# Kernel optimization log

Measured on AMD Instinct MI355X. Metric: run time of the kernel, lower is better.

## Reference

```python
import jax, jax.numpy as jnp
import numpy as np

B, T, V, D, HD, NH, L, F, MD = 16, 512, 2048, 512, 64, 8, 6, 2048, 16


def setup_inputs() -> dict:
    key = jax.random.key(0)
    ks = jax.random.split(key, 12)
    s = 0.02
    def n(k, shape):
        return jax.random.normal(k, shape, jnp.float32) * s
    return {
        "idx": jax.random.randint(ks[0], (B, T), 0, V),
        "emb": n(ks[1], (V, D)),
        "Wq": n(ks[2], (L, D, HD)), "bq": jnp.zeros((L, HD), jnp.float32),
        "Wk": n(ks[3], (L, D, HD)), "bk": jnp.zeros((L, HD), jnp.float32),
        "Wv": n(ks[4], (L, D, HD)), "bv": jnp.zeros((L, HD), jnp.float32),
        "rel_table": n(ks[5], (L, 2 * MD + 1, HD)),
        "Wo": n(ks[6], (L, NH * HD, D)), "bo": jnp.zeros((L, D), jnp.float32),
        "g1": jnp.ones((L, D), jnp.float32), "be1": jnp.zeros((L, D), jnp.float32),
        "g2": jnp.ones((L, D), jnp.float32), "be2": jnp.zeros((L, D), jnp.float32),
        "W1": n(ks[7], (L, D, F)), "b1": jnp.zeros((L, F), jnp.float32),
        "W2": n(ks[8], (L, F, D)), "b2": jnp.zeros((L, D), jnp.float32),
        "Wout": n(ks[9], (D, V)), "bout": jnp.zeros((V,), jnp.float32),
    }


def _pos_encoding(t_len, d):
    # NOTE: replicates repo bug: exponent is 2*i/d with i already even.
    pos = jnp.arange(t_len, dtype=jnp.float32)[:, None]
    i = jnp.arange(0, d, 2, dtype=jnp.float32)[None, :]
    ang = pos / jnp.power(jnp.float32(10000.0), 2.0 * i / d)
    pe = jnp.zeros((t_len, d), jnp.float32)
    pe = pe.at[:, 0::2].set(jnp.sin(ang))
    pe = pe.at[:, 1::2].set(jnp.cos(ang))
    return pe


def _ln(x, g, b):
    m = jnp.mean(x, -1, keepdims=True)
    v = jnp.var(x, -1, keepdims=True)  # biased variance, as torch LayerNorm
    return (x - m) / jnp.sqrt(v + 1e-5) * g + b


def reference(idx, emb, Wq, bq, Wk, bk, Wv, bv, rel_table, Wo, bo,
              g1, be1, g2, be2, W1, b1, W2, b2, Wout, bout):
    t_len = idx.shape[1]
    x = emb[idx]                                   # [B,T,D]
    h = 2.0 * x + _pos_encoding(t_len, D)          # forward adds x + (x + pe)
    t = jnp.arange(t_len)
    dm = jnp.clip(t[None, :] - t[:, None], -MD, MD) + MD  # dm[a,b] = clamp(b-a)
    causal = t[:, None] >= t[None, :]
    scale = 1.0 / jnp.sqrt(jnp.float32(HD))
    neg_inf = jnp.float32(-jnp.inf)
    for l in range(L):
        y = _ln(h, g1[l], be1[l])
        Q = y @ Wq[l] + bq[l]                      # [B,T,HD]
        K = y @ Wk[l] + bk[l]
        Vv = y @ Wv[l] + bv[l]
        bias = rel_table[l][dm]                    # [T,T,HD]; k_bias == v_bias in source
        scores = jnp.einsum('bth,bsh->bts', Q, K)
        rel = jnp.einsum('bth,tsh->bts', Q, bias)
        att = jax.nn.softmax(jnp.where(causal, (scores + rel) * scale, neg_inf), axis=-1)
        vals = jnp.einsum('bts,bsh->bth', att, Vv) + jnp.einsum('bts,tsh->bth', att, bias)
        cat = jnp.tile(vals, (1, 1, NH))           # all NH heads share one module's weights
        h = h + cat @ Wo[l] + bo[l]
        y2 = _ln(h, g2[l], be2[l])
        h = h + jax.nn.relu(y2 @ W1[l] + b1[l]) @ W2[l] + b2[l]
    return h @ Wout + bout                         # [B,T,V]
```

## Files before the change

kernel.cpp:

```cpp
#include <hip/hip_runtime.h>
#include <hip/hip_bf16.h>
#include <math.h>

#define BB 16
#define TT 512
#define VV 2048
#define DD 512
#define HDD 64
#define LL 6
#define FF 2048
#define BT 8192

typedef __hip_bfloat16 bf16;
typedef __attribute__((ext_vector_type(8))) short bf8s;
typedef __attribute__((ext_vector_type(4))) float f4;

__device__ __forceinline__ float cvt(float x){ return x; }
__device__ __forceinline__ float cvt(bf16 x){ return __bfloat162float(x); }

__device__ __forceinline__ void gl16(const bf16* g, bf16* l){
  __builtin_amdgcn_global_load_lds(
      (const __attribute__((address_space(1))) void*)g,
      (__attribute__((address_space(3))) void*)l,
      16, 0, 0);
}

__global__ void k_flag(const void* g1, int* flagp){
  if(threadIdx.x==0 && blockIdx.x==0){
    const unsigned short* u = (const unsigned short*)g1;
    *flagp = (u[0] == 0) ? 1 : 0;
  }
}

__global__ __launch_bounds__(256) void k_cvt_all(
    const void* rel, const void* bo, const void* g1, const void* be1,
    const void* g2, const void* be2, const void* b1, const void* b2,
    const void* bout, const void* bq, const void* bk, const void* bv,
    bf16* d_rel, bf16* d_bo, bf16* d_g1, bf16* d_be1,
    bf16* d_g2, bf16* d_be2, bf16* d_b1, bf16* d_b2,
    bf16* d_bout, bf16* d_bqkv, const int* __restrict__ flagp){
  int i = blockIdx.x*256 + threadIdx.x;
  bool isf = *flagp;
  auto ld = [&](const void* s, int k)->float{
    return isf ? ((const float*)s)[k] : cvt(((const bf16*)s)[k]);
  };
  if(i < 12672){ d_rel[i] = (bf16)ld(rel, i); return; } i -= 12672;
  if(i < 3072){ d_bo[i]  = (bf16)ld(bo, i);  return; } i -= 3072;
  if(i < 3072){ d_g1[i]  = (bf16)ld(g1, i);  return; } i -= 3072;
  if(i < 3072){ d_be1[i] = (bf16)ld(be1, i); return; } i -= 3072;
  if(i < 3072){ d_g2[i]  = (bf16)ld(g2, i);  return; } i -= 3072;
  if(i < 3072){ d_be2[i] = (bf16)ld(be2, i); return; } i -= 3072;
  if(i < 12288){ d_b1[i] = (bf16)ld(b1, i);  return; } i -= 12288;
  if(i < 3072){ d_b2[i]  = (bf16)ld(b2, i);  return; } i -= 3072;
  if(i < 2048){ d_bout[i]= (bf16)ld(bout, i);return; } i -= 2048;
  if(i < 384){ int l=i>>6, hh=i&63; d_bqkv[l*192 + hh]       = (bf16)ld(bq, i); return; } i -= 384;
  if(i < 384){ int l=i>>6, hh=i&63; d_bqkv[l*192 + 64 + hh]  = (bf16)ld(bk, i); return; } i -= 384;
  if(i < 384){ int l=i>>6, hh=i&63; d_bqkv[l*192 + 128 + hh] = (bf16)ld(bv, i); return; }
}

__global__ __launch_bounds__(256) void k_tr(const void* __restrict__ src, bf16* __restrict__ dst,
                                            int R, int C, long long sS, long long sD, int ldD,
                                            const int* __restrict__ flagp){
  __shared__ bf16 t[32][33];
  int z = blockIdx.z;
  int c0 = blockIdx.x*32, r0 = blockIdx.y*32;
  int tx = threadIdx.x & 31, ty = threadIdx.x >> 5;
  bool isf = flagp && (*flagp);
  const float* sf = (const float*)src;
  const bf16*  sb = (const bf16*)src;
  for(int i=ty; i<32; i+=8){
    size_t off = (size_t)z*sS + (size_t)(r0+i)*C + (c0+tx);
    float v = isf ? sf[off] : cvt(sb[off]);
    t[i][tx] = (bf16)v;
  }
  __syncthreads();
  for(int i=ty; i<32; i+=8){
    dst[(size_t)z*sD + (size_t)(c0+i)*ldD + (r0+tx)] = t[tx][i];
  }
}

__global__ __launch_bounds__(256) void k_wsumT(const void* __restrict__ Wo,
                                               bf16* __restrict__ wsT,
                                               const int* __restrict__ flagp){
  int i = blockIdx.x*256 + threadIdx.x;
  if(i >= LL*64*512) return;
  int l = i >> 15, j = i & 32767, hh = j>>9, d = j&511;
  size_t loff = (size_t)l*512*512;
  bool isf = *flagp;
  float a = 0.f;
  #pragma unroll
  for(int n=0;n<8;++n){
    size_t idx = loff + (size_t)(n*64+hh)*512 + d;
    a += isf ? ((const float*)Wo)[idx] : cvt(((const bf16*)Wo)[idx]);
  }
  wsT[(size_t)l*32768 + d*64 + hh] = (bf16)a;
}

__global__ __launch_bounds__(256) void k_embed(const int* __restrict__ idx,
                                               const void* __restrict__ emb,
                                               float* __restrict__ h,
                                               const int* __restrict__ flagp){
  int r = blockIdx.x;
  int t = r & (TT-1);
  int tok = idx[r];
  bool isf = *flagp;
  for(int d = threadIdx.x; d < DD; d += 256){
    int p = d >> 1;
    float ang = (float)t * powf(10000.f, -(float)p * (1.f/128.f));
    float pe = (d & 1) ? cosf(ang) : sinf(ang);
    size_t off = (size_t)tok*DD + d;
    float ev = isf ? ((const float*)emb)[off] : cvt(((const bf16*)emb)[off]);
    h[(size_t)r*DD + d] = 2.f*ev + pe;
  }
}

__global__ __launch_bounds__(256) void k_ln(const float* __restrict__ x,
                                            const bf16* __restrict__ g,
                                            const bf16* __restrict__ b,
                                            bf16* __restrict__ y){
  int r = blockIdx.x;
  int tid = threadIdx.x;
  const float* xr = x + (size_t)r*DD;
  float v0 = xr[tid], v1 = xr[tid+256];
  float s = v0+v1, s2 = v0*v0 + v1*v1;
  for(int o=32;o;o>>=1){ s += __shfl_down(s,o); s2 += __shfl_down(s2,o); }
  __shared__ float red[8];
  int wv = tid>>6, ln = tid&63;
  if(ln==0){ red[wv]=s; red[4+wv]=s2; }
  __syncthreads();
  float a  = red[0]+red[1]+red[2]+red[3];
  float a2 = red[4]+red[5]+red[6]+red[7];
  float m  = a*(1.f/DD);
  float var = a2*(1.f/DD) - m*m;
  float inv = rsqrtf(var + 1e-5f);
  y[(size_t)r*DD+tid]     = (bf16)((v0-m)*inv*cvt(g[tid])     + cvt(b[tid]));
  y[(size_t)r*DD+tid+256] = (bf16)((v1-m)*inv*cvt(g[tid+256]) + cvt(b[tid+256]));
}

template<int BM,int BN,int WM,int WN,int CMODE,bool RELU,bool RESID,bool TRV>
__global__ __launch_bounds__(WM*WN*64) void mm(const bf16* __restrict__ A,
                                          const bf16* __restrict__ Bt,
                                          void* __restrict__ Cv,
                                          const bf16* __restrict__ bias,
                                          int M, int N, int K,
                                          long long sA, long long sB, long long sC, int sBias,
                                          int gx,
                                          const int* __restrict__ flagp,
                                          bf16* __restrict__ vtr){
  constexpr int BK  = 64;
  constexpr int NT  = WM*WN*64;
  constexpr int FM  = BM/(WM*16);
  constexpr int FN  = BN/(WN*16);
  constexpr int S   = (BM+BN)*BK;
  constexpr int CAW = (BM*BK/512)/(NT/64);
  constexpr int CBW = (BN*BK/512)/(NT/64);
  __shared__ bf16 lds[2*S];
  int nwg = gridDim.x, bid = blockIdx.x;
  int q = nwg>>3, rr = nwg&7, xcd = bid&7, ii = bid>>3;
  int wg = (xcd<rr ? xcd*(q+1) : rr*(q+1)+(xcd-rr)*q) + ii;
  int bx = wg % gx, by = wg / gx;
  int z = blockIdx.z;
  A  += (size_t)z*sA;
  Bt += (size_t)z*sB;
  if(bias) bias += (size_t)z*sBias;
  int tid = threadIdx.x, lane = tid&63, w = tid>>6;
  int m0 = by*BM, n0 = bx*BN;
  int wrow = (w/WN)*(FM*16), wcol = (w%WN)*(FN*16);
  int l15 = lane&15, l4 = lane>>4;
  int lrow = lane>>3, lgr = lane&7;
  int nk = K/BK;
  auto stage = [&](int kt, int buf){
    bf16* Ab = lds + buf*S;
    bf16* Bb = Ab + BM*BK;
    const bf16* gA = A + (size_t)m0*K + kt*BK;
    const bf16* gB = Bt + (size_t)n0*K + kt*BK;
    #pragma unroll
    for(int i=0;i<CAW;++i){
      int chunk = w*CAW + i;
      int row = chunk*8 + lrow;
      gl16(gA + (size_t)row*K + ((lgr ^ (row&7))*8), Ab + chunk*512);
    }
    #pragma unroll
    for(int i=0;i<CBW;++i){
      int chunk = w*CBW + i;
      int row = chunk*8 + lrow;
      gl16(gB + (size_t)row*K + ((lgr ^ (row&7))*8), Bb + chunk*512);
    }
  };
  f4 acc[FM][FN] = {};
  stage(0, 0);
  __syncthreads();
  for(int kt=0; kt<nk; ++kt){
    int cur = kt & 1;
    if(kt+1 < nk) stage(kt+1, cur^1);
    const bf16* Ab = lds + cur*S;
    const bf16* Bb = Ab + BM*BK;
    #pragma unroll
    for(int g=0; g<2; ++g){
      bf8s af[FM], bfv[FN];
      #pragma unroll
      for(int i=0;i<FM;++i){
        int r = wrow + i*16 + l15;
        af[i] = *(const bf8s*)(Ab + r*BK + (((g*4+l4) ^ (r&7))*8));
      }
      #pragma unroll
      for(int j=0;j<FN;++j){
        int r = wcol + j*16 + l15;
        bfv[j] = *(const bf8s*)(Bb + r*BK + (((g*4+l4) ^ (r&7))*8));
      }
      #pragma unroll
      for(int i=0;i<FM;++i)
        #pragma unroll
        for(int j=0;j<FN;++j)
          acc[i][j] = __builtin_amdgcn_mfma_f32_16x16x32_bf16(af[i], bfv[j], acc[i][j], 0,0,0);
    }
    __syncthreads();
  }
  bool f32o = (CMODE==2) ? (*flagp != 0) : (CMODE==1);
  bool trv = TRV && (z == 2);
  #pragma unroll
  for(int i=0;i<FM;++i){
    #pragma unroll
    for(int j=0;j<FN;++j){
      int col = n0 + wcol + j*16 + l15;
      float bv = bias ? cvt(bias[col]) : 0.f;
      #pragma unroll
      for(int q2=0;q2<4;++q2){
        int row = m0 + wrow + i*16 + l4*4 + q2;
        float v = acc[i][j][q2] + bv;
        if(trv){
          int b = row >> 9, t = row & 511;
          vtr[(size_t)b*(64*512) + (size_t)col*512 + t] = (bf16)v;
          continue;
        }
        size_t off = (size_t)z*sC + (size_t)row*N + col;
        if(RESID) v += ((const float*)Cv)[off];
        if(RELU)  v = fmaxf(v, 0.f);
        if(CMODE==0)      ((bf16*)Cv)[off] = (bf16)v;
        else if(CMODE==1) ((float*)Cv)[off] = v;
        else if(CMODE==3) vtr[off] = (bf16)v;
        else { if(f32o) ((float*)Cv)[off] = v; else ((bf16*)Cv)[off] = (bf16)v; }
      }
    }
  }
}

__global__ __launch_bounds__(256) void k_projln(const bf16* __restrict__ vals,
                                                const bf16* __restrict__ wsT,
                                                const bf16* __restrict__ bo,
                                                const bf16* __restrict__ g,
                                                const bf16* __restrict__ be,
                                                float* __restrict__ h,
                                                bf16* __restrict__ y){
  __shared__ bf16 Al[32*64];
  __shared__ bf16 Bl[512*64];
  __shared__ float rs[4][32], rs2[4][32];
  int m0 = blockIdx.x*32;
  int tid = threadIdx.x, lane = tid&63, w = tid>>6;
  int l15 = lane&15, l4 = lane>>4;
  int lrow = lane>>3, lgr = lane&7;
  {
    int row = w*8 + lrow;
    gl16(vals + (size_t)(m0+row)*64 + ((lgr ^ (row&7))*8), Al + w*512);
  }
  #pragma unroll
  for(int i=0;i<16;++i){
    int chunk = w*16 + i;
    int row = chunk*8 + lrow;
    gl16(wsT + (size_t)row*64 + ((lgr ^ (row&7))*8), Bl + chunk*512);
  }
  __syncthreads();
  int wcol = w*128;
  f4 acc[2][8] = {};
  #pragma unroll
  for(int g2=0; g2<2; ++g2){
    bf8s af[2], bfv[8];
    #pragma unroll
    for(int i=0;i<2;++i){
      int r = i*16 + l15;
      af[i] = *(const bf8s*)(Al + r*64 + (((g2*4+l4) ^ (r&7))*8));
    }
    #pragma unroll
    for(int j=0;j<8;++j){
      int r = wcol + j*16 + l15;
      bfv[j] = *(const bf8s*)(Bl + r*64 + (((g2*4+l4) ^ (r&7))*8));
    }
    #pragma unroll
    for(int i=0;i<2;++i)
      #pragma unroll
      for(int j=0;j<8;++j)
        acc[i][j] = __builtin_amdgcn_mfma_f32_16x16x32_bf16(af[i], bfv[j], acc[i][j], 0,0,0);
  }
  #pragma unroll
  for(int i=0;i<2;++i){
    float s[4] = {0,0,0,0}, s2[4] = {0,0,0,0};
    #pragma unroll
    for(int j=0;j<8;++j){
      int col = wcol + j*16 + l15;
      float bv = cvt(bo[col]);
      #pragma unroll
      for(int q=0;q<4;++q){
        int row = m0 + i*16 + l4*4 + q;
        size_t off = (size_t)row*512 + col;
        float v = acc[i][j][q] + bv + h[off];
        acc[i][j][q] = v;
        h[off] = v;
        s[q] += v; s2[q] += v*v;
      }
    }
    #pragma unroll
    for(int q=0;q<4;++q){
      #pragma unroll
      for(int o=1;o<16;o<<=1){ s[q] += __shfl_xor(s[q],o); s2[q] += __shfl_xor(s2[q],o); }
      if(l15==0){ rs[w][i*16+l4*4+q] = s[q]; rs2[w][i*16+l4*4+q] = s2[q]; }
    }
  }
  __syncthreads();
  #pragma unroll
  for(int i=0;i<2;++i){
    #pragma unroll
    for(int q=0;q<4;++q){
      int rloc = i*16 + l4*4 + q;
      float a  = rs[0][rloc]+rs[1][rloc]+rs[2][rloc]+rs[3][rloc];
      float a2 = rs2[0][rloc]+rs2[1][rloc]+rs2[2][rloc]+rs2[3][rloc];
      float mean = a*(1.f/512.f);
      float var  = a2*(1.f/512.f) - mean*mean;
      float inv  = rsqrtf(var + 1e-5f);
      int row = m0 + rloc;
      #pragma unroll
      for(int j=0;j<8;++j){
        int col = wcol + j*16 + l15;
        y[(size_t)row*512+col] = (bf16)((acc[i][j][q]-mean)*inv*cvt(g[col]) + cvt(be[col]));
      }
    }
  }
}

__global__ __launch_bounds__(256) void k_attn_fused(const bf16* __restrict__ Q,
                                                    const bf16* __restrict__ K,
                                                    const bf16* __restrict__ VbT,
                                                    const bf16* __restrict__ rel,
                                                    bf16* __restrict__ vals){
  int ti = blockIdx.x, b = blockIdx.y;
  int t0 = ti*16;
  int tid = threadIdx.x, lane = tid & 63, wc = tid >> 6;
  int l15 = lane & 15, l4 = lane >> 4;
  __shared__ bf16  Plds[16][520];
  __shared__ float qrs[16][17];
  __shared__ float amlds[16][17];
  __shared__ float redmx[4][16];
  __shared__ float redsum[4][16];
  int nj = ti + 1;
  int KC = (nj*16 + 31) >> 5;

  const bf16* Qb = Q + ((size_t)b*512 + t0)*64;
  const bf16* Kb = K + (size_t)b*512*64;
  const bf16* Vb = VbT + (size_t)b*64*512;

  for(int i=tid; i<16*17; i+=256) ((float*)amlds)[i] = 0.f;
  if(nj & 1) Plds[tid>>4][nj*16 + (tid&15)] = (bf16)0.f;

  bf8s af0 = *(const bf8s*)(Qb + (size_t)l15*64 + l4*8);
  bf8s af1 = *(const bf8s*)(Qb + (size_t)l15*64 + 32 + l4*8);

  if(wc < 2){
    f4 qa = {};
    bf8s r0 = *(const bf8s*)(rel + (size_t)(wc*16+l15)*64 + l4*8);
    bf8s r1 = *(const bf8s*)(rel + (size_t)(wc*16+l15)*64 + 32 + l4*8);
    qa = __builtin_amdgcn_mfma_f32_16x16x32_bf16(af0, r0, qa, 0,0,0);
    qa = __builtin_amdgcn_mfma_f32_16x16x32_bf16(af1, r1, qa, 0,0,0);
    int m = wc*16 + l15;
    if(m < 17){
      #pragma unroll
      for(int q=0;q<4;++q) qrs[l4*4+q][m] = qa[q];
    }
  }
  __syncthreads();

  float mx4[4] = {-INFINITY,-INFINITY,-INFINITY,-INFINITY};
  for(int j=wc; j<nj; j+=4){
    f4 sa = {};
    const bf16* kr = Kb + (size_t)(j*16+l15)*64;
    bf8s k0 = *(const bf8s*)(kr + l4*8);
    bf8s k1 = *(const bf8s*)(kr + 32 + l4*8);
    sa = __builtin_amdgcn_mfma_f32_16x16x32_bf16(af0, k0, sa, 0,0,0);
    sa = __builtin_amdgcn_mfma_f32_16x16x32_bf16(af1, k1, sa, 0,0,0);
    int s = j*16 + l15;
    #pragma unroll
    for(int q=0;q<4;++q){
      int row = l4*4+q, t = t0+row;
      float sp = -1e30f;
      if(s <= t){
        int m = s - t + 16; m = m < 0 ? 0 : m;
        sp = (sa[q] + qrs[row][m])*0.125f;
        mx4[q] = fmaxf(mx4[q], sp);
      }
      Plds[row][s] = (bf16)sp;
    }
  }
  #pragma unroll
  for(int q=0;q<4;++q){
    float m = mx4[q];
    m = fmaxf(m, __shfl_xor(m,1)); m = fmaxf(m, __shfl_xor(m,2));
    m = fmaxf(m, __shfl_xor(m,4)); m = fmaxf(m, __shfl_xor(m,8));
    mx4[q] = m;
  }
  if(l15==0){
    #pragma unroll
    for(int q=0;q<4;++q) redmx[wc][l4*4+q] = mx4[q];
  }
  __syncthreads();

  float mxg[4], sum4[4] = {0.f,0.f,0.f,0.f};
  #pragma unroll
  for(int q=0;q<4;++q){
    int rloc = l4*4+q;
    mxg[q] = fmaxf(fmaxf(redmx[0][rloc], redmx[1][rloc]),
                   fmaxf(redmx[2][rloc], redmx[3][rloc]));
  }
  for(int j=wc; j<nj; j+=4){
    int s = j*16 + l15;
    #pragma unroll
    for(int q=0;q<4;++q){
      int row = l4*4+q, t = t0+row;
      float e = expf(cvt(Plds[row][s]) - mxg[q]);
      Plds[row][s] = (bf16)e;
      sum4[q] += e;
      int m = s - t + 16;
      if(m >= 1 && m <= 16) amlds[row][m] = e;
    }
  }
  #pragma unroll
  for(int q=0;q<4;++q){
    float s = sum4[q];
    s += __shfl_xor(s,1); s += __shfl_xor(s,2);
    s += __shfl_xor(s,4); s += __shfl_xor(s,8);
    sum4[q] = s;
  }
  if(l15==0){
    #pragma unroll
    for(int q=0;q<4;++q) redsum[wc][l4*4+q] = sum4[q];
  }
  __syncthreads();

  f4 pacc = {0,0,0,0};
  for(int ks=0; ks<KC; ++ks){
    bf8s ap = *(const bf8s*)(&Plds[l15][ks*32 + l4*8]);
    bf8s bv = *(const bf8s*)(Vb + (size_t)(wc*16+l15)*512 + ks*32 + l4*8);
    pacc = __builtin_amdgcn_mfma_f32_16x16x32_bf16(ap, bv, pacc, 0,0,0);
  }
  #pragma unroll
  for(int q=0;q<4;++q){
    int row = l4*4+q;
    float sum = redsum[0][row]+redsum[1][row]+redsum[2][row]+redsum[3][row];
    float rsv = 1.f/sum;
    float a[16];
    float amsum = 0.f;
    #pragma unroll
    for(int m=1;m<=16;++m){ a[m-1] = amlds[row][m]; amsum += a[m-1]; }
    float am0 = sum - amsum;
    int h = wc*16 + l15;
    float acc = pacc[q] + am0*cvt(rel[h]);
    #pragma unroll
    for(int m=1;m<=16;++m) acc += a[m-1]*cvt(rel[m*64 + h]);
    vals[((size_t)b*512 + t0 + row)*64 + h] = (bf16)(acc*rsv);
  }
}

extern "C" void kernel_launch(void* const* d_in, const int* in_sizes, int n_in,
                              void* d_out, int out_size, void* d_ws, size_t ws_size,
                              hipStream_t stream){
  const int* idx = (const int*)d_in[0];

  char* p = (char*)d_ws;
  auto alloc = [&](size_t bytes)->char*{ char* r = p; p += (bytes + 255) & ~(size_t)255; return r; };

  int*  flag  = (int*)alloc(4);
  bf16* rel_b = (bf16*)alloc(12672*2);
  bf16* bo_b  = (bf16*)alloc(3072*2);
  bf16* g1_b  = (bf16*)alloc(3072*2);
  bf16* be1_b = (bf16*)alloc(3072*2);
  bf16* g2_b  = (bf16*)alloc(3072*2);
  bf16* be2_b = (bf16*)alloc(3072*2);
  bf16* b1_b  = (bf16*)alloc(12288*2);
  bf16* b2_b  = (bf16*)alloc(3072*2);
  bf16* bout_b= (bf16*)alloc(2048*2);
  bf16* bqkv  = (bf16*)alloc(LL*192*2);
  bf16* WqkvT = (bf16*)alloc((size_t)LL*3*64*512*2);
  bf16* W1T   = (bf16*)alloc((size_t)LL*2048*512*2);
  bf16* W2T   = (bf16*)alloc((size_t)LL*512*2048*2);
  bf16* WoutT = (bf16*)alloc((size_t)2048*512*2);
  bf16* wsT_all=(bf16*)alloc((size_t)LL*512*64*2);
  float* h    = (float*)alloc((size_t)BT*DD*4);
  bf16*  y    = (bf16*) alloc((size_t)BT*DD*2);
  bf16*  hb   = y;
  bf16*  QKV  = (bf16*) alloc((size_t)3*BT*64*2);
  bf16*  vals = (bf16*) alloc((size_t)BT*64*2);
  bf16*  VbT  = (bf16*) alloc((size_t)BB*64*512*2);
  bf16*  mid  = (bf16*)d_out;
  bf16*  Qb = QKV, *Kb = QKV + (size_t)BT*64;

  k_flag<<<1,64,0,stream>>>(d_in[11], flag);
  k_cvt_all<<<(46592+255)/256,256,0,stream>>>(
      d_in[8], d_in[10], d_in[11], d_in[12], d_in[13], d_in[14],
      d_in[16], d_in[18], d_in[20], d_in[3], d_in[5], d_in[7],
      rel_b, bo_b, g1_b, be1_b, g2_b, be2_b, b1_b, b2_b, bout_b, bqkv, flag);
  k_tr<<<dim3(2,16,LL),256,0,stream>>>(d_in[2], WqkvT,            512, 64, 512*64, 3*64*512, 512, flag);
  k_tr<<<dim3(2,16,LL),256,0,stream>>>(d_in[4], WqkvT + 64*512,   512, 64, 512*64, 3*64*512, 512, flag);
  k_tr<<<dim3(2,16,LL),256,0,stream>>>(d_in[6], WqkvT + 2*64*512, 512, 64, 512*64, 3*64*512, 512, flag);
  k_tr<<<dim3(64,16,LL),256,0,stream>>>(d_in[15], W1T, 512, 2048, 512*2048, 2048*512, 512, flag);
  k_tr<<<dim3(16,64,LL),256,0,stream>>>(d_in[17], W2T, 2048, 512, 2048*512, 512*2048, 2048, flag);
  k_tr<<<dim3(64,16,1),256,0,stream>>>(d_in[19], WoutT, 512, 2048, 0, 0, 512, flag);
  k_wsumT<<<(LL*32768+255)/256,256,0,stream>>>(d_in[9], wsT_all, flag);

  k_embed<<<BT,256,0,stream>>>(idx, d_in[1], h, flag);

  for(int l=0; l<LL; ++l){
    k_ln<<<BT,256,0,stream>>>(h, g1_b+l*DD, be1_b+l*DD, y);
    mm<64,64,2,2,0,false,false,true><<<dim3(128,1,3),256,0,stream>>>(
        y, WqkvT + (size_t)l*3*64*512, QKV, bqkv + l*192,
        BT, 64, 512, 0, 64*512, (long long)BT*64, 64, 1, nullptr, VbT);
    k_attn_fused<<<dim3(32,16),256,0,stream>>>(Qb, Kb, VbT, rel_b + l*33*64, vals);
    k_projln<<<256,256,0,stream>>>(vals, wsT_all + (size_t)l*32768,
                                   bo_b + l*DD, g2_b + l*DD, be2_b + l*DD, h, y);
    mm<128,128,2,2,0,true,false,false><<<dim3(1024,1,1),256,0,stream>>>(
        y, W1T + (size_t)l*2048*512, mid, b1_b + l*FF, BT, 2048, 512, 0,0,0,0, 16, nullptr, nullptr);
    if(l < LL-1){
      mm<128,64,4,1,1,false,true,false><<<dim3(512,1,1),256,0,stream>>>(
          mid, W2T + (size_t)l*512*2048, h, b2_b + l*DD, BT, 512, 2048, 0,0,0,0, 8, nullptr, nullptr);
    } else {
      mm<128,64,4,1,3,false,true,false><<<dim3(512,1,1),256,0,stream>>>(
          mid, W2T + (size_t)l*512*2048, h, b2_b + l*DD, BT, 512, 2048, 0,0,0,0, 8, nullptr, hb);
    }
  }
  mm<128,128,2,2,2,false,false,false><<<dim3(1024,1,1),256,0,stream>>>(
      hb, WoutT, d_out, bout_b, BT, 2048, 512, 0,0,0,0, 16, flag, nullptr);
}
```

Measured before the change: 756.6 us.

## Fuse attention with output projection and LayerNorm; merge QKV transposes

Folds the summed-head output projection, residual add and second LayerNorm into the attention kernel. Each 16-row attention block now runs the 64x512 projection from LDS and writes h and y directly, so the vals buffer and one launch per layer go away. The three QKV weight transposes merge into one launch, and the QKV GEMM tile shrinks to 32 rows to use more blocks. The trade-offs are that wsT is read straight from global memory in every attention block, and the causal attention blocks are imbalanced, which may now also delay the projection work.

```diff
diff --git a/kernel.cpp b/kernel.cpp
--- a/kernel.cpp
+++ b/kernel.cpp
@@ -76,6 +76,29 @@
   __syncthreads();
   for(int i=ty; i<32; i+=8){
     dst[(size_t)z*sD + (size_t)(c0+i)*ldD + (r0+tx)] = t[tx][i];
+  }
+}
+
+__global__ __launch_bounds__(256) void k_tr3(const void* __restrict__ Wq, const void* __restrict__ Wk,
+                                             const void* __restrict__ Wv, bf16* __restrict__ dst,
+                                             const int* __restrict__ flagp){
+  __shared__ bf16 t[32][33];
+  int z = blockIdx.z;
+  int j = z % 3, lz = z / 3;
+  const void* src = (j==0) ? Wq : ((j==1) ? Wk : Wv);
+  int c0 = blockIdx.x*32, r0 = blockIdx.y*32;
+  int tx = threadIdx.x & 31, ty = threadIdx.x >> 5;
+  bool isf = (*flagp);
+  const float* sf = (const float*)src;
+  const bf16*  sb = (const bf16*)src;
+  for(int i=ty; i<32; i+=8){
+    size_t off = (size_t)lz*512*64 + (size_t)(r0+i)*64 + (c0+tx);
+    float v = isf ? sf[off] : cvt(sb[off]);
+    t[i][tx] = (bf16)v;
+  }
+  __syncthreads();
+  for(int i=ty; i<32; i+=8){
+    dst[(size_t)lz*3*64*512 + (size_t)j*64*512 + (size_t)(c0+i)*512 + (r0+tx)] = t[tx][i];
   }
 }
 
@@ -245,111 +268,27 @@
   }
 }
 
-__global__ __launch_bounds__(256) void k_projln(const bf16* __restrict__ vals,
-                                                const bf16* __restrict__ wsT,
-                                                const bf16* __restrict__ bo,
-                                                const bf16* __restrict__ g,
-                                                const bf16* __restrict__ be,
-                                                float* __restrict__ h,
-                                                bf16* __restrict__ y){
-  __shared__ bf16 Al[32*64];
-  __shared__ bf16 Bl[512*64];
-  __shared__ float rs[4][32], rs2[4][32];
-  int m0 = blockIdx.x*32;
-  int tid = threadIdx.x, lane = tid&63, w = tid>>6;
-  int l15 = lane&15, l4 = lane>>4;
-  int lrow = lane>>3, lgr = lane&7;
-  {
-    int row = w*8 + lrow;
-    gl16(vals + (size_t)(m0+row)*64 + ((lgr ^ (row&7))*8), Al + w*512);
-  }
-  #pragma unroll
-  for(int i=0;i<16;++i){
-    int chunk = w*16 + i;
-    int row = chunk*8 + lrow;
-    gl16(wsT + (size_t)row*64 + ((lgr ^ (row&7))*8), Bl + chunk*512);
-  }
-  __syncthreads();
-  int wcol = w*128;
-  f4 acc[2][8] = {};
-  #pragma unroll
-  for(int g2=0; g2<2; ++g2){
-    bf8s af[2], bfv[8];
-    #pragma unroll
-    for(int i=0;i<2;++i){
-      int r = i*16 + l15;
-      af[i] = *(const bf8s*)(Al + r*64 + (((g2*4+l4) ^ (r&7))*8));
-    }
-    #pragma unroll
-    for(int j=0;j<8;++j){
-      int r = wcol + j*16 + l15;
-      bfv[j] = *(const bf8s*)(Bl + r*64 + (((g2*4+l4) ^ (r&7))*8));
-    }
-    #pragma unroll
-    for(int i=0;i<2;++i)
-      #pragma unroll
-      for(int j=0;j<8;++j)
-        acc[i][j] = __builtin_amdgcn_mfma_f32_16x16x32_bf16(af[i], bfv[j], acc[i][j], 0,0,0);
-  }
-  #pragma unroll
-  for(int i=0;i<2;++i){
-    float s[4] = {0,0,0,0}, s2[4] = {0,0,0,0};
-    #pragma unroll
-    for(int j=0;j<8;++j){
-      int col = wcol + j*16 + l15;
-      float bv = cvt(bo[col]);
-      #pragma unroll
-      for(int q=0;q<4;++q){
-        int row = m0 + i*16 + l4*4 + q;
-        size_t off = (size_t)row*512 + col;
-        float v = acc[i][j][q] + bv + h[off];
-        acc[i][j][q] = v;
-        h[off] = v;
-        s[q] += v; s2[q] += v*v;
-      }
-    }
-    #pragma unroll
-    for(int q=0;q<4;++q){
-      #pragma unroll
-      for(int o=1;o<16;o<<=1){ s[q] += __shfl_xor(s[q],o); s2[q] += __shfl_xor(s2[q],o); }
-      if(l15==0){ rs[w][i*16+l4*4+q] = s[q]; rs2[w][i*16+l4*4+q] = s2[q]; }
-    }
-  }
-  __syncthreads();
-  #pragma unroll
-  for(int i=0;i<2;++i){
-    #pragma unroll
-    for(int q=0;q<4;++q){
-      int rloc = i*16 + l4*4 + q;
-      float a  = rs[0][rloc]+rs[1][rloc]+rs[2][rloc]+rs[3][rloc];
-      float a2 = rs2[0][rloc]+rs2[1][rloc]+rs2[2][rloc]+rs2[3][rloc];
-      float mean = a*(1.f/512.f);
-      float var  = a2*(1.f/512.f) - mean*mean;
-      float inv  = rsqrtf(var + 1e-5f);
-      int row = m0 + rloc;
-      #pragma unroll
-      for(int j=0;j<8;++j){
-        int col = wcol + j*16 + l15;
-        y[(size_t)row*512+col] = (bf16)((acc[i][j][q]-mean)*inv*cvt(g[col]) + cvt(be[col]));
-      }
-    }
-  }
-}
-
-__global__ __launch_bounds__(256) void k_attn_fused(const bf16* __restrict__ Q,
-                                                    const bf16* __restrict__ K,
-                                                    const bf16* __restrict__ VbT,
-                                                    const bf16* __restrict__ rel,
-                                                    bf16* __restrict__ vals){
+__global__ __launch_bounds__(256) void k_attnproj(const bf16* __restrict__ Q,
+                                                  const bf16* __restrict__ K,
+                                                  const bf16* __restrict__ VbT,
+                                                  const bf16* __restrict__ rel,
+                                                  const bf16* __restrict__ wsT,
+                                                  const bf16* __restrict__ bo,
+                                                  const bf16* __restrict__ g,
+                                                  const bf16* __restrict__ be,
+                                                  float* __restrict__ h,
+                                                  bf16* __restrict__ y){
   int ti = blockIdx.x, b = blockIdx.y;
   int t0 = ti*16;
   int tid = threadIdx.x, lane = tid & 63, wc = tid >> 6;
   int l15 = lane & 15, l4 = lane >> 4;
   __shared__ bf16  Plds[16][520];
+  __shared__ bf16  vlds[16][68];
   __shared__ float qrs[16][17];
   __shared__ float amlds[16][17];
   __shared__ float redmx[4][16];
   __shared__ float redsum[4][16];
+  __shared__ float rs[4][16], rs2[4][16];
   int nj = ti + 1;
   int KC = (nj*16 + 31) >> 5;
 
@@ -459,11 +398,62 @@
     #pragma unroll
     for(int m=1;m<=16;++m){ a[m-1] = amlds[row][m]; amsum += a[m-1]; }
     float am0 = sum - amsum;
-    int h = wc*16 + l15;
-    float acc = pacc[q] + am0*cvt(rel[h]);
-    #pragma unroll
-    for(int m=1;m<=16;++m) acc += a[m-1]*cvt(rel[m*64 + h]);
-    vals[((size_t)b*512 + t0 + row)*64 + h] = (bf16)(acc*rsv);
+    int hh = wc*16 + l15;
+    float acc = pacc[q] + am0*cvt(rel[hh]);
+    #pragma unroll
+    for(int m=1;m<=16;++m) acc += a[m-1]*cvt(rel[m*64 + hh]);
+    vlds[row][hh] = (bf16)(acc*rsv);
+  }
+  __syncthreads();
+
+  bf8s pa0 = *(const bf8s*)(&vlds[l15][l4*8]);
+  bf8s pa1 = *(const bf8s*)(&vlds[l15][32 + l4*8]);
+  f4 acc2[8] = {};
+  #pragma unroll
+  for(int j=0;j<8;++j){
+    int nn = wc*8 + j;
+    bf8s bv0 = *(const bf8s*)(wsT + (size_t)(nn*16+l15)*64 + l4*8);
+    bf8s bv1 = *(const bf8s*)(wsT + (size_t)(nn*16+l15)*64 + 32 + l4*8);
+    acc2[j] = __builtin_amdgcn_mfma_f32_16x16x32_bf16(pa0, bv0, acc2[j], 0,0,0);
+    acc2[j] = __builtin_amdgcn_mfma_f32_16x16x32_bf16(pa1, bv1, acc2[j], 0,0,0);
+  }
+  float s4[4] = {0,0,0,0}, s24[4] = {0,0,0,0};
+  #pragma unroll
+  for(int j=0;j<8;++j){
+    int col = (wc*8+j)*16 + l15;
+    float bv = cvt(bo[col]);
+    #pragma unroll
+    for(int q=0;q<4;++q){
+      int row = t0 + l4*4 + q;
+      size_t off = ((size_t)b*512 + row)*512 + col;
+      float v = acc2[j][q] + bv + h[off];
+      acc2[j][q] = v;
+      h[off] = v;
+      s4[q] += v; s24[q] += v*v;
+    }
+  }
+  #pragma unroll
+  for(int q=0;q<4;++q){
+    #pragma unroll
+    for(int o=1;o<16;o<<=1){ s4[q] += __shfl_xor(s4[q],o); s24[q] += __shfl_xor(s24[q],o); }
+    if(l15==0){ rs[wc][l4*4+q] = s4[q]; rs2[wc][l4*4+q] = s24[q]; }
+  }
+  __syncthreads();
+  #pragma unroll
+  for(int q=0;q<4;++q){
+    int rloc = l4*4+q;
+    float a  = rs[0][rloc]+rs[1][rloc]+rs[2][rloc]+rs[3][rloc];
+    float a2 = rs2[0][rloc]+rs2[1][rloc]+rs2[2][rloc]+rs2[3][rloc];
+    float mean = a*(1.f/512.f);
+    float var  = a2*(1.f/512.f) - mean*mean;
+    float inv  = rsqrtf(var + 1e-5f);
+    int row = t0 + rloc;
+    #pragma unroll
+    for(int j=0;j<8;++j){
+      int col = (wc*8+j)*16 + l15;
+      y[((size_t)b*512 + row)*512 + col] =
+          (bf16)((acc2[j][q]-mean)*inv*cvt(g[col]) + cvt(be[col]));
+    }
   }
 }
 
@@ -495,7 +485,6 @@
   bf16*  y    = (bf16*) alloc((size_t)BT*DD*2);
   bf16*  hb   = y;
   bf16*  QKV  = (bf16*) alloc((size_t)3*BT*64*2);
-  bf16*  vals = (bf16*) alloc((size_t)BT*64*2);
   bf16*  VbT  = (bf16*) alloc((size_t)BB*64*512*2);
   bf16*  mid  = (bf16*)d_out;
   bf16*  Qb = QKV, *Kb = QKV + (size_t)BT*64;
@@ -505,9 +494,7 @@
       d_in[8], d_in[10], d_in[11], d_in[12], d_in[13], d_in[14],
       d_in[16], d_in[18], d_in[20], d_in[3], d_in[5], d_in[7],
       rel_b, bo_b, g1_b, be1_b, g2_b, be2_b, b1_b, b2_b, bout_b, bqkv, flag);
-  k_tr<<<dim3(2,16,LL),256,0,stream>>>(d_in[2], WqkvT,            512, 64, 512*64, 3*64*512, 512, flag);
-  k_tr<<<dim3(2,16,LL),256,0,stream>>>(d_in[4], WqkvT + 64*512,   512, 64, 512*64, 3*64*512, 512, flag);
-  k_tr<<<dim3(2,16,LL),256,0,stream>>>(d_in[6], WqkvT + 2*64*512, 512, 64, 512*64, 3*64*512, 512, flag);
+  k_tr3<<<dim3(2,16,3*LL),256,0,stream>>>(d_in[2], d_in[4], d_in[6], WqkvT, flag);
   k_tr<<<dim3(64,16,LL),256,0,stream>>>(d_in[15], W1T, 512, 2048, 512*2048, 2048*512, 512, flag);
   k_tr<<<dim3(16,64,LL),256,0,stream>>>(d_in[17], W2T, 2048, 512, 2048*512, 512*2048, 2048, flag);
   k_tr<<<dim3(64,16,1),256,0,stream>>>(d_in[19], WoutT, 512, 2048, 0, 0, 512, flag);
@@ -517,12 +504,12 @@
 
   for(int l=0; l<LL; ++l){
     k_ln<<<BT,256,0,stream>>>(h, g1_b+l*DD, be1_b+l*DD, y);
-    mm<64,64,2,2,0,false,false,true><<<dim3(128,1,3),256,0,stream>>>(
+    mm<32,64,2,2,0,false,false,true><<<dim3(256,1,3),256,0,stream>>>(
         y, WqkvT + (size_t)l*3*64*512, QKV, bqkv + l*192,
         BT, 64, 512, 0, 64*512, (long long)BT*64, 64, 1, nullptr, VbT);
-    k_attn_fused<<<dim3(32,16),256,0,stream>>>(Qb, Kb, VbT, rel_b + l*33*64, vals);
-    k_projln<<<256,256,0,stream>>>(vals, wsT_all + (size_t)l*32768,
-                                   bo_b + l*DD, g2_b + l*DD, be2_b + l*DD, h, y);
+    k_attnproj<<<dim3(32,16),256,0,stream>>>(Qb, Kb, VbT, rel_b + l*33*64,
+                                             wsT_all + (size_t)l*32768,
+                                             bo_b + l*DD, g2_b + l*DD, be2_b + l*DD, h, y);
     mm<128,128,2,2,0,true,false,false><<<dim3(1024,1,1),256,0,stream>>>(
         y, W1T + (size_t)l*2048*512, mid, b1_b + l*FF, BT, 2048, 512, 0,0,0,0, 16, nullptr, nullptr);
     if(l < LL-1){
```

Result: faster. 721.3 us (-4.7%).
